# Performance work log

Hardware: AMD Instinct MI355X
Metric: run time of the kernel (lower is better)

The kernel has to match this reference:

```python
import jax, jax.numpy as jnp
import numpy as np

def setup_inputs() -> dict:
    key = jax.random.key(0)
    kq, kk, kv = jax.random.split(key, 3)
    S, D = 4096, 512
    q = jax.random.normal(kq, (S, D), dtype=jnp.float32)
    k = jax.random.normal(kk, (S, D), dtype=jnp.float32)
    v = jax.random.normal(kv, (S, D), dtype=jnp.float32)
    return {"q": q, "k": k, "v": v}

def reference(q, k, v):
    # scaled dot-product attention, unmasked (mask_future=False path)
    d = q.shape[-1]
    scores = jnp.einsum('sd,td->st', q, k) / jnp.sqrt(jnp.asarray(d, q.dtype))
    attn = jax.nn.softmax(scores, axis=-1)
    return jnp.einsum('st,td->sd', attn, v)
```

## Files before the change

### kernel.cpp

```cpp
#include <hip/hip_runtime.h>
#include <hip/hip_bf16.h>

#define SEQ 4096
#define DIM 512
#define SCALE 0.044194173824159216f

#define SPLITS 4
#define BQ 64
#define KVBLK 64
#define KEYS_PER_SPLIT (SEQ / SPLITS)
#define ITERS (KEYS_PER_SPLIT / KVBLK)
#define THR_DEFER 8.0f

typedef __attribute__((ext_vector_type(8))) short short8;
typedef __attribute__((ext_vector_type(4))) float f32x4;
typedef __attribute__((ext_vector_type(16))) float f32x16;

__device__ __forceinline__ short f2bf(float f) {
  union { float f; unsigned u; } c; c.f = f;
  unsigned u = c.u;
  return (short)((u + 0x7FFFu + ((u >> 16) & 1u)) >> 16);
}

__device__ __forceinline__ float bf2f(unsigned short b) {
  union { unsigned u; float f; } c;
  c.u = ((unsigned)b) << 16;
  return c.f;
}

__device__ __forceinline__ short8 pack8(float4 a, float4 b) {
  short8 r;
  r[0] = f2bf(a.x); r[1] = f2bf(a.y); r[2] = f2bf(a.z); r[3] = f2bf(a.w);
  r[4] = f2bf(b.x); r[5] = f2bf(b.y); r[6] = f2bf(b.z); r[7] = f2bf(b.w);
  return r;
}

__device__ __forceinline__ ushort4 pack4(float a, float b, float c, float d) {
  ushort4 r;
  r.x = (unsigned short)f2bf(a); r.y = (unsigned short)f2bf(b);
  r.z = (unsigned short)f2bf(c); r.w = (unsigned short)f2bf(d);
  return r;
}

__device__ __forceinline__ void gload16(const void* g, void* l) {
  __builtin_amdgcn_global_load_lds(
      (const __attribute__((address_space(1))) unsigned int*)g,
      (__attribute__((address_space(3))) unsigned int*)l, 16, 0, 0);
}

__global__ void prep_fused(const float* __restrict__ k, ushort* __restrict__ kbf,
                           const float* __restrict__ q, ushort* __restrict__ qbf,
                           const float* __restrict__ v, ushort* __restrict__ vt) {
  __shared__ float t[64][65];
  const int tid = threadIdx.x;
  if (blockIdx.x < 1024) {
    int i = blockIdx.x * 256 + tid;
    const float4* p = (const float4*)(k + (size_t)i * 8);
    *(short8*)(kbf + (size_t)i * 8) = pack8(p[0], p[1]);
    return;
  }
  if (blockIdx.x < 2048) {
    int i = (blockIdx.x - 1024) * 256 + tid;
    const float4* p = (const float4*)(q + (size_t)i * 8);
    *(short8*)(qbf + (size_t)i * 8) = pack8(p[0], p[1]);
    return;
  }
  const int bid = blockIdx.x - 2048;
  const int bs = bid % (SEQ / 64);
  const int bd = bid / (SEQ / 64);
  const int s0 = bs * 64, d0 = bd * 64;
#pragma unroll
  for (int kk = 0; kk < 16; ++kk) {
    int idx = kk * 256 + tid;
    int r = idx >> 6, c = idx & 63;
    t[r][c] = v[(size_t)(s0 + r) * DIM + d0 + c];
  }
  __syncthreads();
#pragma unroll
  for (int kk = 0; kk < 16; ++kk) {
    int idx = kk * 256 + tid;
    int dr = idx >> 6, sc = idx & 63;
    vt[(size_t)(d0 + dr) * SEQ + s0 + sc] = (ushort)f2bf(t[sc][dr]);
  }
}

__global__ __launch_bounds__(512, 2) void attn_split(
    const ushort* __restrict__ qbf, const ushort* __restrict__ kbf,
    const ushort* __restrict__ vt, ushort* __restrict__ opart,
    float* __restrict__ ml) {
  __shared__ __align__(16) ushort kt[KVBLK * DIM];
  __shared__ __align__(16) ushort vtt[DIM * KVBLK];
  __shared__ __align__(16) ushort p_lds[BQ * KVBLK];
  __shared__ float mx_st[2][BQ];
  __shared__ float osc_st[BQ];
  __shared__ float l_st[2][BQ];
  __shared__ int   flag_st[4];

  const int tid  = threadIdx.x;
  const int lane = tid & 63;
  const int w    = tid >> 6;
  const int lr   = lane & 15;
  const int lg   = lane >> 4;
  const int l31  = lane & 31;
  const int hi   = lane >> 5;
  const int sp   = blockIdx.x & (SPLITS - 1);
  const int qb   = blockIdx.x >> 2;
  const int rg   = w & 3;
  const int kh   = w >> 2;
  const int rg_pv = w & 1;
  const int cg    = w >> 1;
  const int qrow0 = qb * BQ;
  const int kbase = sp * KEYS_PER_SPLIT;

  short8 qf[16];
  {
    const ushort* qp = qbf + (size_t)(qrow0 + rg * 16 + lr) * DIM + lg * 8;
#pragma unroll
    for (int c = 0; c < 16; ++c)
      qf[c] = *(const short8*)(qp + c * 32);
  }
  f32x16 oacc[4] = {};
  float m_reg = -INFINITY, l_reg = 0.f;

  auto stageK = [&](int kb) {
#pragma unroll
    for (int i = 0; i < 8; ++i) {
      int r = w * 8 + i;
      const ushort* src = kbf + (size_t)(kb + r) * DIM + ((lane ^ (r & 31)) * 8);
      gload16(src, &kt[r * DIM]);
    }
  };
  auto stageV = [&](int kb) {
#pragma unroll
    for (int j = 0; j < 8; ++j) {
      int r0 = w * 64 + j * 8;
      int rr = r0 + (lane >> 3);
      const ushort* src = vt + (size_t)rr * SEQ + kb + (((lane & 7) ^ (rr & 7)) * 8);
      gload16(src, &vtt[r0 * KVBLK]);
    }
  };

  stageK(kbase);

#pragma unroll 1
  for (int it = 0; it < ITERS; ++it) {
    const int kb = kbase + it * KVBLK;

    asm volatile("s_waitcnt vmcnt(0)" ::: "memory");
    __builtin_amdgcn_s_barrier();

    stageV(kb);

    f32x4 s0 = {}, s1 = {};
    {
      const int kr0 = kh * 32 + lr;
      const int kr1 = kr0 + 16;
      const char* kb0 = (const char*)kt + kr0 * 1024;
      const char* kb1 = (const char*)kt + kr1 * 1024;
      const int sw0 = kr0 & 31, sw1 = kr1 & 31;
      __builtin_amdgcn_s_setprio(1);
#pragma unroll
      for (int c = 0; c < 16; ++c) {
        short8 k0 = *(const short8*)(kb0 + (((c * 4 + lg) ^ sw0) << 4));
        short8 k1 = *(const short8*)(kb1 + (((c * 4 + lg) ^ sw1) << 4));
        s0 = __builtin_amdgcn_mfma_f32_16x16x32_bf16(k0, qf[c], s0, 0, 0, 0);
        s1 = __builtin_amdgcn_mfma_f32_16x16x32_bf16(k1, qf[c], s1, 0, 0, 0);
      }
      __builtin_amdgcn_s_setprio(0);
    }

    float sc0[4], sc1[4];
#pragma unroll
    for (int r = 0; r < 4; ++r) { sc0[r] = s0[r] * SCALE; sc1[r] = s1[r] * SCALE; }
    float tmax = fmaxf(fmaxf(fmaxf(sc0[0], sc0[1]), fmaxf(sc0[2], sc0[3])),
                       fmaxf(fmaxf(sc1[0], sc1[1]), fmaxf(sc1[2], sc1[3])));
    tmax = fmaxf(tmax, __shfl_xor(tmax, 16));
    tmax = fmaxf(tmax, __shfl_xor(tmax, 32));
    if (lane < 16) mx_st[kh][rg * 16 + lane] = tmax;

    asm volatile("s_waitcnt lgkmcnt(0)" ::: "memory");
    __builtin_amdgcn_s_barrier();

    if (it + 1 < ITERS) stageK(kb + KVBLK);

    {
      const int row = rg * 16 + lr;
      float tmax64 = fmaxf(mx_st[0][row], mx_st[1][row]);
      bool resc = tmax64 > m_reg + THR_DEFER;
      float mnew = resc ? tmax64 : m_reg;
      float osc = __expf(m_reg - mnew);
      unsigned long long bl = __ballot(resc);
      if (kh == 0 && lane == 0) flag_st[rg] = (bl != 0ull) ? 1 : 0;
      if (kh == 0 && lane < 16) osc_st[row] = osc;
      m_reg = mnew;
      l_reg *= osc;
      float p0[4], p1[4];
#pragma unroll
      for (int r = 0; r < 4; ++r) {
        p0[r] = __expf(sc0[r] - m_reg);
        p1[r] = __expf(sc1[r] - m_reg);
      }
      float ps = ((p0[0] + p0[1]) + (p0[2] + p0[3])) +
                 ((p1[0] + p1[1]) + (p1[2] + p1[3]));
      ps += __shfl_xor(ps, 16);
      ps += __shfl_xor(ps, 32);
      l_reg += ps;
      char* pb = (char*)p_lds + row * 128;
      const int sw = (row & 7) << 4;
      const int off = kh * 64 + lg * 8;
      *(ushort4*)(pb + (off ^ sw))        = pack4(p0[0], p0[1], p0[2], p0[3]);
      *(ushort4*)(pb + ((off + 32) ^ sw)) = pack4(p1[0], p1[1], p1[2], p1[3]);
    }

    if (it + 1 < ITERS) {
      asm volatile("s_waitcnt vmcnt(8)" ::: "memory");
    } else {
      asm volatile("s_waitcnt vmcnt(0)" ::: "memory");
    }
    asm volatile("s_waitcnt lgkmcnt(0)" ::: "memory");
    __builtin_amdgcn_s_barrier();

    {
      if (flag_st[rg_pv * 2] | flag_st[rg_pv * 2 + 1]) {
        float ov[16];
#pragma unroll
        for (int r = 0; r < 16; ++r)
          ov[r] = osc_st[rg_pv * 32 + (r & 3) + 8 * (r >> 2) + 4 * hi];
#pragma unroll
        for (int t = 0; t < 4; ++t)
#pragma unroll
          for (int r = 0; r < 16; ++r) oacc[t][r] *= ov[r];
      }
      const int arow = rg_pv * 32 + l31;
      const char* prow = (const char*)p_lds + arow * 128;
      const int psw = (arow & 7) << 4;
      __builtin_amdgcn_s_setprio(1);
#pragma unroll
      for (int c = 0; c < 4; ++c) {
        short8 pa = *(const short8*)(prow + ((c * 32 + hi * 16) ^ psw));
#pragma unroll
        for (int t = 0; t < 4; ++t) {
          int vrow = cg * 128 + t * 32 + l31;
          short8 vf = *(const short8*)((const char*)vtt + vrow * 128 +
                                       ((c * 32 + hi * 16) ^ ((vrow & 7) << 4)));
          oacc[t] = __builtin_amdgcn_mfma_f32_32x32x16_bf16(pa, vf, oacc[t], 0, 0, 0);
        }
      }
      __builtin_amdgcn_s_setprio(0);
    }
  }

  if (lane < 16) {
    l_st[kh][rg * 16 + lane] = l_reg;
    if (kh == 0) mx_st[0][rg * 16 + lane] = m_reg;
  }
  __syncthreads();
  {
    ushort* op = opart + ((size_t)sp * SEQ + qrow0 + rg_pv * 32) * DIM + cg * 128;
#pragma unroll
    for (int t = 0; t < 4; ++t)
#pragma unroll
      for (int r = 0; r < 16; ++r) {
        int crow = (r & 3) + 8 * (r >> 2) + 4 * hi;
        op[(size_t)crow * DIM + t * 32 + l31] = (ushort)f2bf(oacc[t][r]);
      }
  }
  if (tid < BQ) {
    size_t base = ((size_t)sp * SEQ + qrow0 + tid) * 2;
    ml[base]     = mx_st[0][tid];
    ml[base + 1] = l_st[0][tid] + l_st[1][tid];
  }
}

__global__ void combine(const ushort* __restrict__ opart, const float* __restrict__ ml,
                        float* __restrict__ out) {
  int gid = blockIdx.x * 256 + threadIdx.x;
  int row = gid >> 6;
  int dv  = (gid & 63) * 8;
  float m[SPLITS], l[SPLITS], wgt[SPLITS];
  float M = -INFINITY;
#pragma unroll
  for (int i = 0; i < SPLITS; ++i) {
    m[i] = ml[((size_t)i * SEQ + row) * 2];
    l[i] = ml[((size_t)i * SEQ + row) * 2 + 1];
    M = fmaxf(M, m[i]);
  }
  float L = 0.f;
#pragma unroll
  for (int i = 0; i < SPLITS; ++i) { wgt[i] = __expf(m[i] - M); L += l[i] * wgt[i]; }
  float inv = 1.f / L;
  float acc[8] = {};
#pragma unroll
  for (int i = 0; i < SPLITS; ++i) {
    short8 o = *(const short8*)(opart + ((size_t)i * SEQ + row) * DIM + dv);
#pragma unroll
    for (int j = 0; j < 8; ++j) acc[j] += bf2f((unsigned short)o[j]) * wgt[i];
  }
  float4 r0, r1;
  r0.x = acc[0] * inv; r0.y = acc[1] * inv; r0.z = acc[2] * inv; r0.w = acc[3] * inv;
  r1.x = acc[4] * inv; r1.y = acc[5] * inv; r1.z = acc[6] * inv; r1.w = acc[7] * inv;
  *(float4*)(out + (size_t)row * DIM + dv)     = r0;
  *(float4*)(out + (size_t)row * DIM + dv + 4) = r1;
}

__global__ __launch_bounds__(512) void attn_fused_fb(
    const float* __restrict__ q, const float* __restrict__ k,
    const float* __restrict__ v, float* __restrict__ out) {
  __shared__ float s_lds[16][128];
  __shared__ __align__(16) unsigned short p_lds[16 * 128];
  __shared__ float m_st[16], l_st[16], osc_st[16];
  const int tid = threadIdx.x, lane = tid & 63, w = tid >> 6;
  const int lr = lane & 15, lg = lane >> 4, qb = blockIdx.x * 16;
  if (tid < 16) { m_st[tid] = -INFINITY; l_st[tid] = 0.f; }
  short8 qf[16];
  {
    const float* qp = q + (size_t)(qb + lr) * DIM + lg * 8;
#pragma unroll
    for (int c = 0; c < 16; ++c)
      qf[c] = pack8(*(const float4*)(qp + c * 32), *(const float4*)(qp + c * 32 + 4));
  }
  f32x4 oacc[4] = {};
  __syncthreads();
  for (int it = 0; it < SEQ / 128; ++it) {
    const int kb = it * 128;
    {
      const float* kp = k + (size_t)(kb + w * 16 + lr) * DIM + lg * 8;
      f32x4 sacc = {};
#pragma unroll
      for (int c = 0; c < 16; ++c) {
        short8 kf = pack8(*(const float4*)(kp + c * 32), *(const float4*)(kp + c * 32 + 4));
        sacc = __builtin_amdgcn_mfma_f32_16x16x32_bf16(qf[c], kf, sacc, 0, 0, 0);
      }
#pragma unroll
      for (int r = 0; r < 4; ++r) s_lds[lg * 4 + r][w * 16 + lr] = sacc[r] * SCALE;
    }
    __syncthreads();
    {
      const int srow = tid >> 5, sj = tid & 31;
      float4 sv = *(const float4*)&s_lds[srow][sj * 4];
      float tmax = fmaxf(fmaxf(sv.x, sv.y), fmaxf(sv.z, sv.w));
#pragma unroll
      for (int m = 16; m >= 1; m >>= 1) tmax = fmaxf(tmax, __shfl_xor(tmax, m));
      float mold = m_st[srow], mnew = fmaxf(mold, tmax);
      float p0 = __expf(sv.x - mnew), p1 = __expf(sv.y - mnew);
      float p2 = __expf(sv.z - mnew), p3 = __expf(sv.w - mnew);
      float psum = (p0 + p1) + (p2 + p3);
#pragma unroll
      for (int m = 16; m >= 1; m >>= 1) psum += __shfl_xor(psum, m);
      if (sj == 0) {
        float sc = __expf(mold - mnew);
        l_st[srow] = l_st[srow] * sc + psum; m_st[srow] = mnew; osc_st[srow] = sc;
      }
      ushort4 pb;
      pb.x = (unsigned short)f2bf(p0); pb.y = (unsigned short)f2bf(p1);
      pb.z = (unsigned short)f2bf(p2); pb.w = (unsigned short)f2bf(p3);
      int lin = srow * 256 + sj * 8;
      *(ushort4*)((char*)p_lds + (lin ^ ((srow & 7) << 4))) = pb;
    }
    __syncthreads();
    {
      float osc[4];
#pragma unroll
      for (int r = 0; r < 4; ++r) osc[r] = osc_st[lg * 4 + r];
#pragma unroll
      for (int ct = 0; ct < 4; ++ct)
#pragma unroll
        for (int r = 0; r < 4; ++r) oacc[ct][r] *= osc[r];
#pragma unroll
      for (int kc = 0; kc < 4; ++kc) {
        int lin = lr * 256 + (kc * 32 + 8 * lg) * 2;
        short8 pf = *(const short8*)((const char*)p_lds + (lin ^ ((lr & 7) << 4)));
        const float* vp0 = v + (size_t)(kb + kc * 32 + 8 * lg) * DIM + w * 64 + lr;
#pragma unroll
        for (int ct = 0; ct < 4; ++ct) {
          const float* vp = vp0 + ct * 16;
          short8 vf;
#pragma unroll
          for (int jj = 0; jj < 8; ++jj) vf[jj] = f2bf(vp[(size_t)jj * DIM]);
          oacc[ct] = __builtin_amdgcn_mfma_f32_16x16x32_bf16(pf, vf, oacc[ct], 0, 0, 0);
        }
      }
    }
    __syncthreads();
  }
  {
    float linv[4];
#pragma unroll
    for (int r = 0; r < 4; ++r) linv[r] = 1.f / l_st[lg * 4 + r];
#pragma unroll
    for (int ct = 0; ct < 4; ++ct)
#pragma unroll
      for (int r = 0; r < 4; ++r)
        out[(size_t)(qb + lg * 4 + r) * DIM + w * 64 + ct * 16 + lr] =
            oacc[ct][r] * linv[r];
  }
}

extern "C" void kernel_launch(void* const* d_in, const int* in_sizes, int n_in,
                              void* d_out, int out_size, void* d_ws, size_t ws_size,
                              hipStream_t stream) {
  (void)in_sizes; (void)n_in; (void)out_size;
  const float* q = (const float*)d_in[0];
  const float* k = (const float*)d_in[1];
  const float* v = (const float*)d_in[2];
  float* out = (float*)d_out;

  const size_t kbf_elems = (size_t)SEQ * DIM;
  const size_t qbf_elems = (size_t)SEQ * DIM;
  const size_t vt_elems  = (size_t)DIM * SEQ;
  const size_t op_elems  = (size_t)SPLITS * SEQ * DIM;
  const size_t ml_elems  = (size_t)SPLITS * SEQ * 2;
  const size_t need = kbf_elems * 2 + qbf_elems * 2 + vt_elems * 2 +
                      op_elems * 2 + ml_elems * 4;

  if (ws_size >= need) {
    ushort* kbf   = (ushort*)d_ws;
    ushort* qbf   = kbf + kbf_elems;
    ushort* vtb   = qbf + qbf_elems;
    ushort* opart = vtb + vt_elems;
    float* ml     = (float*)(opart + op_elems);

    prep_fused<<<2048 + (SEQ / 64) * (DIM / 64), 256, 0, stream>>>(k, kbf, q, qbf, v, vtb);
    attn_split<<<(SEQ / BQ) * SPLITS, 512, 0, stream>>>(qbf, kbf, vtb, opart, ml);
    combine<<<(SEQ * DIM / 8) / 256, 256, 0, stream>>>(opart, ml, out);
  } else {
    attn_fused_fb<<<SEQ / 16, 512, 0, stream>>>(q, k, v, out);
  }
}
```

Measured before the change: 75.13 us.

## Fuse split-KV combine into attention kernel via last-block atomic counter

Removes the separate combine kernel launch. Each attention block increments a per-query-block atomic counter after writing its partial output and stats, and the last of the four split blocks for a query tile performs the log-sum-exp merge and writes the final fp32 output. The counters are zeroed in the prep kernel. This saves one kernel launch and lets combining overlap with other blocks' attention work, at the cost of threadfences, an atomic per block, and serialized combine work inside the tail blocks.

```diff
diff --git a/kernel.cpp b/kernel.cpp
--- a/kernel.cpp
+++ b/kernel.cpp
@@ -11,6 +11,7 @@
 #define KEYS_PER_SPLIT (SEQ / SPLITS)
 #define ITERS (KEYS_PER_SPLIT / KVBLK)
 #define THR_DEFER 8.0f
+#define NQB (SEQ / BQ)
 
 typedef __attribute__((ext_vector_type(8))) short short8;
 typedef __attribute__((ext_vector_type(4))) float f32x4;
@@ -50,10 +51,12 @@
 
 __global__ void prep_fused(const float* __restrict__ k, ushort* __restrict__ kbf,
                            const float* __restrict__ q, ushort* __restrict__ qbf,
-                           const float* __restrict__ v, ushort* __restrict__ vt) {
+                           const float* __restrict__ v, ushort* __restrict__ vt,
+                           int* __restrict__ cnt) {
   __shared__ float t[64][65];
   const int tid = threadIdx.x;
   if (blockIdx.x < 1024) {
+    if (blockIdx.x == 0 && tid < NQB) cnt[tid] = 0;
     int i = blockIdx.x * 256 + tid;
     const float4* p = (const float4*)(k + (size_t)i * 8);
     *(short8*)(kbf + (size_t)i * 8) = pack8(p[0], p[1]);
@@ -87,7 +90,7 @@
 __global__ __launch_bounds__(512, 2) void attn_split(
     const ushort* __restrict__ qbf, const ushort* __restrict__ kbf,
     const ushort* __restrict__ vt, ushort* __restrict__ opart,
-    float* __restrict__ ml) {
+    float* __restrict__ ml, int* __restrict__ cnt, float* __restrict__ out) {
   __shared__ __align__(16) ushort kt[KVBLK * DIM];
   __shared__ __align__(16) ushort vtt[DIM * KVBLK];
   __shared__ __align__(16) ushort p_lds[BQ * KVBLK];
@@ -95,6 +98,7 @@
   __shared__ float osc_st[BQ];
   __shared__ float l_st[2][BQ];
   __shared__ int   flag_st[4];
+  __shared__ int   last_st;
 
   const int tid  = threadIdx.x;
   const int lane = tid & 63;
@@ -270,37 +274,44 @@
     ml[base]     = mx_st[0][tid];
     ml[base + 1] = l_st[0][tid] + l_st[1][tid];
   }
-}
-
-__global__ void combine(const ushort* __restrict__ opart, const float* __restrict__ ml,
-                        float* __restrict__ out) {
-  int gid = blockIdx.x * 256 + threadIdx.x;
-  int row = gid >> 6;
-  int dv  = (gid & 63) * 8;
-  float m[SPLITS], l[SPLITS], wgt[SPLITS];
-  float M = -INFINITY;
-#pragma unroll
-  for (int i = 0; i < SPLITS; ++i) {
-    m[i] = ml[((size_t)i * SEQ + row) * 2];
-    l[i] = ml[((size_t)i * SEQ + row) * 2 + 1];
-    M = fmaxf(M, m[i]);
-  }
-  float L = 0.f;
-#pragma unroll
-  for (int i = 0; i < SPLITS; ++i) { wgt[i] = __expf(m[i] - M); L += l[i] * wgt[i]; }
-  float inv = 1.f / L;
-  float acc[8] = {};
-#pragma unroll
-  for (int i = 0; i < SPLITS; ++i) {
-    short8 o = *(const short8*)(opart + ((size_t)i * SEQ + row) * DIM + dv);
-#pragma unroll
-    for (int j = 0; j < 8; ++j) acc[j] += bf2f((unsigned short)o[j]) * wgt[i];
-  }
-  float4 r0, r1;
-  r0.x = acc[0] * inv; r0.y = acc[1] * inv; r0.z = acc[2] * inv; r0.w = acc[3] * inv;
-  r1.x = acc[4] * inv; r1.y = acc[5] * inv; r1.z = acc[6] * inv; r1.w = acc[7] * inv;
-  *(float4*)(out + (size_t)row * DIM + dv)     = r0;
-  *(float4*)(out + (size_t)row * DIM + dv + 4) = r1;
+
+  __threadfence();
+  __syncthreads();
+  if (tid == 0) last_st = (atomicAdd(&cnt[qb], 1) == SPLITS - 1) ? 1 : 0;
+  __syncthreads();
+  if (last_st) {
+    __threadfence();
+#pragma unroll 1
+    for (int ii = tid; ii < BQ * (DIM / 8); ii += 512) {
+      int row = qrow0 + (ii >> 6);
+      int dv  = (ii & 63) * 8;
+      float m[SPLITS], l[SPLITS], wgt[SPLITS];
+      float M = -INFINITY;
+#pragma unroll
+      for (int i = 0; i < SPLITS; ++i) {
+        m[i] = ml[((size_t)i * SEQ + row) * 2];
+        l[i] = ml[((size_t)i * SEQ + row) * 2 + 1];
+        M = fmaxf(M, m[i]);
+      }
+      float L = 0.f;
+#pragma unroll
+      for (int i = 0; i < SPLITS; ++i) { wgt[i] = __expf(m[i] - M); L += l[i] * wgt[i]; }
+      float inv = 1.f / L;
+      float acc[8] = {};
+#pragma unroll
+      for (int i = 0; i < SPLITS; ++i) {
+        short8 o = *(const short8*)(opart + ((size_t)i * SEQ + row) * DIM + dv);
+#pragma unroll
+        for (int j = 0; j < 8; ++j) acc[j] += bf2f((unsigned short)o[j]) * wgt[i];
+      }
+      float4 r0, r1;
+      r0.x = acc[0] * inv; r0.y = acc[1] * inv; r0.z = acc[2] * inv; r0.w = acc[3] * inv;
+      r1.x = acc[4] * inv; r1.y = acc[5] * inv; r1.z = acc[6] * inv; r1.w = acc[7] * inv;
+      *(float4*)(out + (size_t)row * DIM + dv)     = r0;
+      *(float4*)(out + (size_t)row * DIM + dv + 4) = r1;
+    }
+    if (tid == 0) cnt[qb] = 0;
+  }
 }
 
 __global__ __launch_bounds__(512) void attn_fused_fb(
@@ -411,7 +422,7 @@
   const size_t op_elems  = (size_t)SPLITS * SEQ * DIM;
   const size_t ml_elems  = (size_t)SPLITS * SEQ * 2;
   const size_t need = kbf_elems * 2 + qbf_elems * 2 + vt_elems * 2 +
-                      op_elems * 2 + ml_elems * 4;
+                      op_elems * 2 + ml_elems * 4 + NQB * 4;
 
   if (ws_size >= need) {
     ushort* kbf   = (ushort*)d_ws;
@@ -419,10 +430,10 @@
     ushort* vtb   = qbf + qbf_elems;
     ushort* opart = vtb + vt_elems;
     float* ml     = (float*)(opart + op_elems);
-
-    prep_fused<<<2048 + (SEQ / 64) * (DIM / 64), 256, 0, stream>>>(k, kbf, q, qbf, v, vtb);
-    attn_split<<<(SEQ / BQ) * SPLITS, 512, 0, stream>>>(qbf, kbf, vtb, opart, ml);
-    combine<<<(SEQ * DIM / 8) / 256, 256, 0, stream>>>(opart, ml, out);
+    int* cnt      = (int*)(ml + ml_elems);
+
+    prep_fused<<<2048 + (SEQ / 64) * (DIM / 64), 256, 0, stream>>>(k, kbf, q, qbf, v, vtb, cnt);
+    attn_split<<<(SEQ / BQ) * SPLITS, 512, 0, stream>>>(qbf, kbf, vtb, opart, ml, cnt, out);
   } else {
     attn_fused_fb<<<SEQ / 16, 512, 0, stream>>>(q, k, v, out);
   }
```

Result: slower. 149.3 us (+98.7%).
